# Kernel optimization log

Measured on AMD Instinct MI355X. Metric: run time of the kernel, lower is better.

The kernel has to match this reference:

```python
import jax, jax.numpy as jnp
import numpy as np
from jax import lax

B, T = 64, 200
NUM_C, DIM_S, SIZE_M = 2000, 128, 50


def setup_inputs() -> dict:
    key = jax.random.key(0)
    ks = jax.random.split(key, 12)
    d = {}
    d['skill'] = jax.random.randint(ks[0], (B, T), 0, NUM_C)
    d['answer'] = jax.random.randint(ks[1], (B, T), 0, 2)
    s = 1.0 / np.sqrt(DIM_S)
    d['k_emb'] = jax.random.normal(ks[2], (NUM_C + 1, DIM_S), jnp.float32)
    d['v_emb'] = jax.random.normal(ks[3], (2 * NUM_C + 1, DIM_S), jnp.float32)
    # kaiming_normal on [size_m, dim_s]: std = sqrt(2/dim_s)
    d['Mk'] = jax.random.normal(ks[4], (SIZE_M, DIM_S), jnp.float32) * np.sqrt(2.0 / DIM_S)
    d['Mv0'] = jax.random.normal(ks[5], (SIZE_M, DIM_S), jnp.float32) * np.sqrt(2.0 / DIM_S)
    d['f_W'] = jax.random.normal(ks[6], (DIM_S, 2 * DIM_S), jnp.float32) * (1.0 / np.sqrt(2 * DIM_S))
    d['f_b'] = jnp.zeros((DIM_S,), jnp.float32)
    d['p_W'] = jax.random.normal(ks[7], (NUM_C, DIM_S), jnp.float32) * s
    d['p_b'] = jnp.zeros((NUM_C,), jnp.float32)
    d['e_W'] = jax.random.normal(ks[8], (DIM_S, DIM_S), jnp.float32) * s
    d['e_b'] = jnp.zeros((DIM_S,), jnp.float32)
    d['a_W'] = jax.random.normal(ks[9], (DIM_S, DIM_S), jnp.float32) * s
    d['a_b'] = jnp.zeros((DIM_S,), jnp.float32)
    return d


def reference(skill, answer, k_emb, v_emb, Mk, Mv0, f_W, f_b, p_W, p_b, e_W, e_b, a_W, a_b):
    num_c = p_W.shape[0]
    bsz = skill.shape[0]
    answer_x = jnp.where(answer == 2, 1, answer)
    x = skill + num_c * answer_x                       # [B,T]
    k = k_emb[skill]                                   # [B,T,D]
    v = v_emb[x]                                       # [B,T,D]
    w = jax.nn.softmax(jnp.einsum('btd,md->btm', k, Mk), axis=-1)   # [B,T,M]
    e = jax.nn.sigmoid(jnp.einsum('btd,ed->bte', v, e_W) + e_b)      # [B,T,D]
    a = jnp.tanh(jnp.einsum('btd,ed->bte', v, a_W) + a_b)            # [B,T,D]

    Mv_init = jnp.broadcast_to(Mv0, (bsz,) + Mv0.shape)              # [B,M,D]

    def step(Mvt, inp):
        et, at, wt = inp                               # [B,D],[B,D],[B,M]
        # read uses pre-update memory (Mv[:, :-1] in the torch code)
        read = jnp.einsum('bm,bmd->bd', wt, Mvt)
        Mvt_new = Mvt * (1.0 - wt[:, :, None] * et[:, None, :]) + wt[:, :, None] * at[:, None, :]
        return Mvt_new, read

    _, reads = lax.scan(step, Mv_init,
                        (e.transpose(1, 0, 2), a.transpose(1, 0, 2), w.transpose(1, 0, 2)))
    reads = reads.transpose(1, 0, 2)                   # [B,T,D]

    f = jnp.tanh(jnp.concatenate([reads, k], axis=-1) @ f_W.T + f_b)  # [B,T,D]
    p = jax.nn.sigmoid(f @ p_W.T + p_b)                # [B,T,num_c] (dropout is identity at eval)
    p = p[:, :-1, :]
    next_skill = skill[:, 1:]                          # [B,T-1]
    idx = jnp.minimum(next_skill, num_c - 1)
    pred = jnp.take_along_axis(p, idx[..., None], axis=-1)[..., 0]
    pred = jnp.where(next_skill < num_c, pred, 0.0)    # index num_c -> zero row in torch one_hot
    return pred
```

## Files before the change

kernel.cpp:

```cpp
#include <hip/hip_runtime.h>
#include <math.h>

#define Bsz 64
#define Tn 200
#define NUMC 2000
#define DS 128
#define SM 50
#define NTOK (Bsz*Tn)
#define WVS 10
#define CH 40
#define NCH (Tn/CH)

typedef __attribute__((ext_vector_type(8))) short bfrag;
typedef __attribute__((ext_vector_type(4))) float f32x4;
typedef __attribute__((ext_vector_type(4))) unsigned int u32x4;

__device__ __forceinline__ unsigned short f2bf(float x) {
    unsigned int u = __builtin_bit_cast(unsigned int, x);
    u = u + 0x7fffu + ((u >> 16) & 1u);
    return (unsigned short)(u >> 16);
}
__device__ __forceinline__ unsigned int pack2(float a, float b) {
    return (unsigned int)f2bf(a) | ((unsigned int)f2bf(b) << 16);
}
__device__ __forceinline__ bfrag mk_frag(f32x4 x, f32x4 y) {
    u32x4 t;
    t[0] = pack2(x[0], x[1]); t[1] = pack2(x[2], x[3]);
    t[2] = pack2(y[0], y[1]); t[3] = pack2(y[2], y[3]);
    return __builtin_bit_cast(bfrag, t);
}

__device__ __forceinline__ float fast_exp(float x)  { return __builtin_amdgcn_exp2f(x * 1.44269504f); }
__device__ __forceinline__ float fast_rcp(float x)  { return __builtin_amdgcn_rcpf(x); }
__device__ __forceinline__ float fast_sigmoid(float x) { return fast_rcp(1.f + fast_exp(-x)); }
__device__ __forceinline__ float fast_tanh(float x) { return 1.f - 2.f * fast_rcp(fast_exp(2.f * x) + 1.f); }

__global__ __launch_bounds__(256) void k0_cast(
    const float* __restrict__ eW, const float* __restrict__ aW,
    const float* __restrict__ fW, const float* __restrict__ Mk,
    unsigned int* __restrict__ BeaU, unsigned int* __restrict__ BkmU,
    unsigned int* __restrict__ Bf0U)
{
    const int g = blockIdx.x * 256 + threadIdx.x;
    if (g >= 9216) return;
    int gm, mat;
    unsigned int* dst;
    if (g < 4096)      { mat = 0; gm = g;        dst = BeaU; }
    else if (g < 7168) { mat = 1; gm = g - 4096; dst = BkmU; }
    else               { mat = 2; gm = g - 7168; dst = Bf0U; }
    const int nt = gm >> 8, r = gm & 255, ki = r >> 6, L = r & 63;
    const int n = nt * 16 + (L & 15);
    const int k = ki * 32 + (L >> 4) * 8;

    const float* src = nullptr;
    if (mat == 0) {
        src = (n < 128) ? (eW + (size_t)n * DS + k) : (aW + (size_t)(n - 128) * DS + k);
    } else if (mat == 1) {
        if (n < 128)      src = fW + (size_t)n * (2 * DS) + DS + k;
        else if (n < 128 + SM) src = Mk + (size_t)(n - 128) * DS + k;
    } else {
        src = fW + (size_t)n * (2 * DS) + k;
    }
    float v[8];
    #pragma unroll
    for (int j = 0; j < 8; j++) v[j] = src ? src[j] : 0.f;
    u32x4 o;
    o[0] = pack2(v[0], v[1]); o[1] = pack2(v[2], v[3]);
    o[2] = pack2(v[4], v[5]); o[3] = pack2(v[6], v[7]);
    ((u32x4*)dst)[gm] = o;
}

__global__ __launch_bounds__(64, 4) void k1_gemm(
    const int* __restrict__ skill, const int* __restrict__ answer,
    const float* __restrict__ k_emb, const float* __restrict__ v_emb,
    const unsigned int* __restrict__ BeaU, const unsigned int* __restrict__ BkmU,
    const float* __restrict__ eB, const float* __restrict__ aB,
    float* __restrict__ w_buf, float* __restrict__ e_buf,
    float* __restrict__ a_buf, float* __restrict__ kp_buf)
{
    const int bid = blockIdx.x;
    const int tile = bid / 7, role = bid % 7;
    const int L = threadIdx.x, L15 = L & 15, quad = L >> 4;
    const int tok0 = tile * 16;
    const int tokA = tok0 + L15;
    const int row0 = tok0 + quad * 4;

    const int s = skill[tokA];
    const float* ap;
    if (role < 4) {
        const int an = answer[tokA];
        const int ax = (an == 2) ? 1 : an;
        ap = v_emb + ((size_t)(s + NUMC * ax)) * DS + quad * 8;
    } else {
        ap = k_emb + (size_t)s * DS + quad * 8;
    }
    bfrag Af[4];
    #pragma unroll
    for (int ki = 0; ki < 4; ki++) {
        const f32x4* a4 = (const f32x4*)(ap + ki * 32);
        Af[ki] = mk_frag(a4[0], a4[1]);
    }

    const bfrag* Bp = (role < 4) ? (const bfrag*)BeaU : (const bfrag*)BkmU;
    const int g0 = (role < 4) ? role * 4 : (role - 4) * 4;

    f32x4 acc[4];
    #pragma unroll
    for (int t = 0; t < 4; t++) acc[t] = (f32x4){0.f,0.f,0.f,0.f};

    #pragma unroll
    for (int half = 0; half < 2; half++) {
        bfrag bh[2][4];
        #pragma unroll
        for (int tt = 0; tt < 2; tt++)
            #pragma unroll
            for (int ki = 0; ki < 4; ki++)
                bh[tt][ki] = Bp[(size_t)((g0 + half * 2 + tt) * 4 + ki) * 64 + L];
        #pragma unroll
        for (int ki = 0; ki < 4; ki++)
            #pragma unroll
            for (int tt = 0; tt < 2; tt++)
                acc[half * 2 + tt] = __builtin_amdgcn_mfma_f32_16x16x32_bf16(
                    Af[ki], bh[tt][ki], acc[half * 2 + tt], 0, 0, 0);
    }

    if (role == 6) {
        #pragma unroll
        for (int reg = 0; reg < 4; reg++) {
            float mx = -1e30f;
            #pragma unroll
            for (int t = 0; t < 4; t++) { const int c = t * 16 + L15; if (c < SM) mx = fmaxf(mx, acc[t][reg]); }
            #pragma unroll
            for (int msk = 1; msk <= 8; msk <<= 1) mx = fmaxf(mx, __shfl_xor(mx, msk));
            float ex[4]; float ssum = 0.f;
            #pragma unroll
            for (int t = 0; t < 4; t++) {
                const int c = t * 16 + L15;
                ex[t] = (c < SM) ? fast_exp(acc[t][reg] - mx) : 0.f;
                ssum += ex[t];
            }
            #pragma unroll
            for (int msk = 1; msk <= 8; msk <<= 1) ssum += __shfl_xor(ssum, msk);
            const float inv = fast_rcp(ssum);
            float* wp = w_buf + (size_t)(row0 + reg) * SM;
            #pragma unroll
            for (int t = 0; t < 4; t++) { const int c = t * 16 + L15; if (c < SM) wp[c] = ex[t] * inv; }
        }
    } else {
        const int nb = (role & 1) * 64;
        float* obuf = (role < 2) ? e_buf : (role < 4) ? a_buf : kp_buf;
        const float* bias = (role < 2) ? eB : aB;
        #pragma unroll
        for (int t = 0; t < 4; t++) {
            const int n = nb + t * 16 + L15;
            const float bv = (role < 4) ? bias[n] : 0.f;
            #pragma unroll
            for (int reg = 0; reg < 4; reg++) {
                float v = acc[t][reg] + bv;
                if (role < 2)      v = fast_sigmoid(v);
                else if (role < 4) v = fast_tanh(v);
                obuf[(size_t)(row0 + reg) * DS + n] = v;
            }
        }
    }
}

__global__ __launch_bounds__(640) void k2_scan(
    const float* __restrict__ w_buf, const float* __restrict__ e_buf,
    const float* __restrict__ a_buf, const float* __restrict__ Mv0,
    unsigned short* __restrict__ reads)
{
    const int bi   = blockIdx.x;
    const int b    = bi >> 1;
    const int dh   = bi & 1;
    const int tid  = threadIdx.x;
    const int wv   = tid >> 6;
    const int L    = tid & 63;
    const int d    = dh * 64 + L;
    const int m0e  = wv * 5;
    const int base = b * Tn;

    __shared__ float se_s[2][CH][64];
    __shared__ float sa_s[2][CH][64];
    __shared__ float sw_s[2][CH * SM];
    __shared__ float red[2][WVS][8][64];

    float Mv[5];
    #pragma unroll
    for (int m = 0; m < 5; m++) Mv[m] = Mv0[(size_t)(m0e + m) * DS + d];

    const int r0 = tid >> 6, c0 = tid & 63;

    {
        const size_t ebase = (size_t)base * DS + dh * 64 + c0;
        #pragma unroll
        for (int pp = 0; pp < 4; pp++) {
            const int row = pp * 10 + r0;
            se_s[0][row][c0] = e_buf[ebase + (size_t)row * DS];
            sa_s[0][row][c0] = a_buf[ebase + (size_t)row * DS];
        }
        const int wbase = base * SM;
        #pragma unroll
        for (int pp = 0; pp < 4; pp++) {
            const int j = tid + pp * 640;
            if (j < CH * SM) sw_s[0][j] = w_buf[wbase + j];
        }
    }
    __syncthreads();

    float se[4][2], sa[4][2], sw[4][2][5];
    int p = 0;

    #define LOADST(ST, TL)                                                     \
        { const int tl_ = (TL);                                                \
          if (tl_ < CH) {                                                      \
            _Pragma("unroll")                                                  \
            for (int q_ = 0; q_ < 2; q_++) {                                   \
                se[ST][q_] = se_s[p][tl_ + q_][L];                             \
                sa[ST][q_] = sa_s[p][tl_ + q_][L];                             \
                _Pragma("unroll")                                              \
                for (int m_ = 0; m_ < 5; m_++)                                 \
                    sw[ST][q_][m_] = sw_s[p][(tl_ + q_) * SM + m0e + m_];      \
            } } }

    for (int c = 0; c < NCH; c++) {
        float st_e[4], st_a[4], st_w[4];
        if (c + 1 < NCH) {
            const int tcn = (c + 1) * CH;
            const size_t ebase = (size_t)(base + tcn) * DS + dh * 64 + c0;
            #pragma unroll
            for (int pp = 0; pp < 4; pp++) {
                const int row = pp * 10 + r0;
                st_e[pp] = e_buf[ebase + (size_t)row * DS];
                st_a[pp] = a_buf[ebase + (size_t)row * DS];
            }
            const int wbase = (base + tcn) * SM;
            #pragma unroll
            for (int pp = 0; pp < 4; pp++) {
                const int j = tid + pp * 640;
                if (j < CH * SM) st_w[pp] = w_buf[wbase + j];
            }
        }

        LOADST(0, 0) LOADST(1, 2) LOADST(2, 4) LOADST(3, 6)

        #pragma unroll 1
        for (int ti = 0; ti < 5; ti++) {
            const int tlb = ti * 8;
            const int gi  = c * 5 + ti;
            const int pr  = gi & 1;
            #pragma unroll
            for (int sub = 0; sub < 4; sub++) {
                #pragma unroll
                for (int q = 0; q < 2; q++) {
                    const float ev = se[sub][q], av = sa[sub][q];
                    float rd = 0.f;
                    #pragma unroll
                    for (int m = 0; m < 5; m++) {
                        const float wm = sw[sub][q][m];
                        rd = fmaf(wm, Mv[m], rd);
                        Mv[m] = fmaf(-wm, fmaf(ev, Mv[m], -av), Mv[m]);
                    }
                    red[pr][wv][sub * 2 + q][L] = rd;
                }
                LOADST(sub, tlb + sub * 2 + 8)
            }
            __syncthreads();
            if (tid < 512) {
                const int tt = tid >> 6, dd = tid & 63;
                float s = red[pr][0][tt][dd];
                #pragma unroll
                for (int g = 1; g < WVS; g++) s += red[pr][g][tt][dd];
                reads[(size_t)(base + c * CH + tlb + tt) * DS + dh * 64 + dd] = f2bf(s);
            }
        }

        if (c + 1 < NCH) {
            #pragma unroll
            for (int pp = 0; pp < 4; pp++) {
                const int row = pp * 10 + r0;
                se_s[p ^ 1][row][c0] = st_e[pp];
                sa_s[p ^ 1][row][c0] = st_a[pp];
            }
            #pragma unroll
            for (int pp = 0; pp < 4; pp++) {
                const int j = tid + pp * 640;
                if (j < CH * SM) sw_s[p ^ 1][j] = st_w[pp];
            }
            __syncthreads();
            p ^= 1;
        }
    }
    #undef LOADST
}

__global__ __launch_bounds__(128, 2) void k3_gemm(
    const unsigned short* __restrict__ reads, const float* __restrict__ kp_buf,
    const unsigned int* __restrict__ Bf0U, const float* __restrict__ fB,
    const float* __restrict__ pW, const float* __restrict__ pB,
    const int* __restrict__ skill, float* __restrict__ out)
{
    const int tid = threadIdx.x;
    const int wv  = tid >> 6;
    const int L   = tid & 63, L15 = L & 15, quad = L >> 4;
    const int tok0 = blockIdx.x * 16;
    const int tokA = tok0 + L15;
    const int row0 = tok0 + quad * 4;

    __shared__ float sm[2][16];

    bfrag Rf[4];
    #pragma unroll
    for (int ki = 0; ki < 4; ki++)
        Rf[ki] = *(const bfrag*)(reads + (size_t)tokA * DS + ki * 32 + quad * 8);

    const bfrag* Bf0 = (const bfrag*)Bf0U;
    const int g0 = wv * 4;

    f32x4 acc[4];
    #pragma unroll
    for (int t = 0; t < 4; t++) acc[t] = (f32x4){0.f,0.f,0.f,0.f};

    #pragma unroll
    for (int half = 0; half < 2; half++) {
        bfrag bh[2][4];
        #pragma unroll
        for (int tt = 0; tt < 2; tt++)
            #pragma unroll
            for (int ki = 0; ki < 4; ki++)
                bh[tt][ki] = Bf0[(size_t)((g0 + half * 2 + tt) * 4 + ki) * 64 + L];
        #pragma unroll
        for (int ki = 0; ki < 4; ki++)
            #pragma unroll
            for (int tt = 0; tt < 2; tt++)
                acc[half * 2 + tt] = __builtin_amdgcn_mfma_f32_16x16x32_bf16(
                    Rf[ki], bh[tt][ki], acc[half * 2 + tt], 0, 0, 0);
    }

    const int nb = wv * 64;
    float f[4][4];
    #pragma unroll
    for (int t = 0; t < 4; t++) {
        const int n = nb + t * 16 + L15;
        const float fb = fB[n];
        #pragma unroll
        for (int reg = 0; reg < 4; reg++)
            f[reg][t] = fast_tanh(acc[t][reg] + kp_buf[(size_t)(row0 + reg) * DS + n] + fb);
    }

    #pragma unroll
    for (int reg = 0; reg < 4; reg++) {
        const int tok = row0 + reg;
        const int t = tok % Tn;
        const bool act = (t < Tn - 1);
        float contrib = 0.f;
        if (act) {
            const int sn = skill[tok + 1];
            const int ix = (sn < NUMC) ? sn : (NUMC - 1);
            const float* pr = pW + (size_t)ix * DS + nb + L15;
            #pragma unroll
            for (int t4 = 0; t4 < 4; t4++)
                contrib = fmaf(f[reg][t4], pr[t4 * 16], contrib);
        }
        #pragma unroll
        for (int msk = 1; msk <= 8; msk <<= 1)
            contrib += __shfl_xor(contrib, msk);
        if (L15 == 0) sm[wv][quad * 4 + reg] = contrib;
    }
    __syncthreads();
    if (tid < 16) {
        const int tok = tok0 + tid;
        const int t = tok % Tn;
        if (t < Tn - 1) {
            const int sn = skill[tok + 1];
            const int ix = (sn < NUMC) ? sn : (NUMC - 1);
            const float val = sm[0][tid] + sm[1][tid] + pB[ix];
            out[(size_t)(tok / Tn) * (Tn - 1) + t] = (sn < NUMC) ? fast_sigmoid(val) : 0.f;
        }
    }
}

extern "C" void kernel_launch(void* const* d_in, const int* in_sizes, int n_in,
                              void* d_out, int out_size, void* d_ws, size_t ws_size,
                              hipStream_t stream)
{
    const int*   skill  = (const int*)  d_in[0];
    const int*   answer = (const int*)  d_in[1];
    const float* k_emb  = (const float*)d_in[2];
    const float* v_emb  = (const float*)d_in[3];
    const float* Mk     = (const float*)d_in[4];
    const float* Mv0    = (const float*)d_in[5];
    const float* f_W    = (const float*)d_in[6];
    const float* f_b    = (const float*)d_in[7];
    const float* p_W    = (const float*)d_in[8];
    const float* p_b    = (const float*)d_in[9];
    const float* e_W    = (const float*)d_in[10];
    const float* e_b    = (const float*)d_in[11];
    const float* a_W    = (const float*)d_in[12];
    const float* a_b    = (const float*)d_in[13];
    float* out = (float*)d_out;

    float* ws     = (float*)d_ws;
    float* w_buf  = ws;
    float* e_buf  = w_buf  + (size_t)NTOK*SM;
    float* a_buf  = e_buf  + (size_t)NTOK*DS;
    float* kp_buf = a_buf  + (size_t)NTOK*DS;
    unsigned short* reads = (unsigned short*)(kp_buf + (size_t)NTOK*DS);
    unsigned int* BeaU = (unsigned int*)(reads + (size_t)NTOK*DS);
    unsigned int* BkmU = BeaU + 4096 * 4;
    unsigned int* Bf0U = BkmU + 3072 * 4;

    k0_cast<<<36, 256, 0, stream>>>(e_W, a_W, f_W, Mk, BeaU, BkmU, Bf0U);
    k1_gemm<<<7*(NTOK/16), 64, 0, stream>>>(skill, answer, k_emb, v_emb,
        BeaU, BkmU, e_b, a_b, w_buf, e_buf, a_buf, kp_buf);
    k2_scan<<<Bsz*2, 640, 0, stream>>>(w_buf, e_buf, a_buf, Mv0, reads);
    k3_gemm<<<NTOK/16, 128, 0, stream>>>(reads, kp_buf, Bf0U, f_b,
        p_W, p_b, skill, out);
}
```

Before: 138.9 us.

## Halve scan block to 5 waves with 10 memory slots each and vectorized LDS

The recurrent scan kernel now uses 320 threads per block, each wave owning 10 memory slots instead of 5. This halves the cross-wave reduction and the number of threads synchronizing each step. Shared buffers are transposed and padded so e, a and w values can be read as vector loads. The reduction also writes packed bf16 pairs. The cost is twice the serial FMA work per thread and more registers per thread.

```diff
diff --git a/kernel.cpp b/kernel.cpp
--- a/kernel.cpp
+++ b/kernel.cpp
@@ -7,12 +7,16 @@
 #define DS 128
 #define SM 50
 #define NTOK (Bsz*Tn)
-#define WVS 10
+#define WVS2 5
+#define MPW 10
 #define CH 40
 #define NCH (Tn/CH)
+#define SEP 44
+#define WROW 60
 
 typedef __attribute__((ext_vector_type(8))) short bfrag;
 typedef __attribute__((ext_vector_type(4))) float f32x4;
+typedef __attribute__((ext_vector_type(2))) float f32x2;
 typedef __attribute__((ext_vector_type(4))) unsigned int u32x4;
 
 __device__ __forceinline__ unsigned short f2bf(float x) {
@@ -165,7 +169,7 @@
     }
 }
 
-__global__ __launch_bounds__(640) void k2_scan(
+__global__ __launch_bounds__(320) void k2_scan(
     const float* __restrict__ w_buf, const float* __restrict__ e_buf,
     const float* __restrict__ a_buf, const float* __restrict__ Mv0,
     unsigned short* __restrict__ reads)
@@ -177,121 +181,130 @@
     const int wv   = tid >> 6;
     const int L    = tid & 63;
     const int d    = dh * 64 + L;
-    const int m0e  = wv * 5;
+    const int m0   = wv * MPW;
     const int base = b * Tn;
 
-    __shared__ float se_s[2][CH][64];
-    __shared__ float sa_s[2][CH][64];
-    __shared__ float sw_s[2][CH * SM];
-    __shared__ float red[2][WVS][8][64];
-
-    float Mv[5];
-    #pragma unroll
-    for (int m = 0; m < 5; m++) Mv[m] = Mv0[(size_t)(m0e + m) * DS + d];
-
-    const int r0 = tid >> 6, c0 = tid & 63;
+    __shared__ __align__(16) float se_s[2][64][SEP];
+    __shared__ __align__(16) float sa_s[2][64][SEP];
+    __shared__ __align__(16) float w_s[2][CH][WROW];
+    __shared__ __align__(16) float red[2][WVS2][8][64];
+
+    float Mv[MPW];
+    #pragma unroll
+    for (int m = 0; m < MPW; m++) Mv[m] = Mv0[(size_t)(m0 + m) * DS + d];
+
+    const int srow = tid >> 6, scol = tid & 63;
 
     {
-        const size_t ebase = (size_t)base * DS + dh * 64 + c0;
-        #pragma unroll
-        for (int pp = 0; pp < 4; pp++) {
-            const int row = pp * 10 + r0;
-            se_s[0][row][c0] = e_buf[ebase + (size_t)row * DS];
-            sa_s[0][row][c0] = a_buf[ebase + (size_t)row * DS];
-        }
-        const int wbase = base * SM;
-        #pragma unroll
-        for (int pp = 0; pp < 4; pp++) {
-            const int j = tid + pp * 640;
-            if (j < CH * SM) sw_s[0][j] = w_buf[wbase + j];
+        #pragma unroll
+        for (int pass = 0; pass < 8; pass++) {
+            const int row = pass * 5 + srow;
+            se_s[0][scol][row] = e_buf[(size_t)(base + row) * DS + dh * 64 + scol];
+            sa_s[0][scol][row] = a_buf[(size_t)(base + row) * DS + dh * 64 + scol];
+        }
+        #pragma unroll
+        for (int pass = 0; pass < 7; pass++) {
+            const int j = tid + pass * 320;
+            if (j < CH * SM) {
+                const int t = j / SM, m = j % SM;
+                w_s[0][t][(m / MPW) * 12 + (m % MPW)] = w_buf[(size_t)base * SM + j];
+            }
         }
     }
     __syncthreads();
 
-    float se[4][2], sa[4][2], sw[4][2][5];
+    f32x4 wlo[2][2], whi[2][2];
+    f32x2 wtl[2][2], sev[2], sav[2];
     int p = 0;
 
-    #define LOADST(ST, TL)                                                     \
+    #define LOADR(SL, TL)                                                      \
         { const int tl_ = (TL);                                                \
           if (tl_ < CH) {                                                      \
+            sev[SL] = *(const f32x2*)&se_s[p][L][tl_];                         \
+            sav[SL] = *(const f32x2*)&sa_s[p][L][tl_];                         \
             _Pragma("unroll")                                                  \
             for (int q_ = 0; q_ < 2; q_++) {                                   \
-                se[ST][q_] = se_s[p][tl_ + q_][L];                             \
-                sa[ST][q_] = sa_s[p][tl_ + q_][L];                             \
-                _Pragma("unroll")                                              \
-                for (int m_ = 0; m_ < 5; m_++)                                 \
-                    sw[ST][q_][m_] = sw_s[p][(tl_ + q_) * SM + m0e + m_];      \
+                const float* wp_ = &w_s[p][tl_ + q_][wv * 12];                 \
+                wlo[SL][q_] = *(const f32x4*)wp_;                              \
+                whi[SL][q_] = *(const f32x4*)(wp_ + 4);                        \
+                wtl[SL][q_] = *(const f32x2*)(wp_ + 8);                        \
             } } }
 
+    LOADR(0, 0) LOADR(1, 2)
+
     for (int c = 0; c < NCH; c++) {
-        float st_e[4], st_a[4], st_w[4];
+        float st_e[8], st_a[8], st_w[7];
         if (c + 1 < NCH) {
-            const int tcn = (c + 1) * CH;
-            const size_t ebase = (size_t)(base + tcn) * DS + dh * 64 + c0;
-            #pragma unroll
-            for (int pp = 0; pp < 4; pp++) {
-                const int row = pp * 10 + r0;
-                st_e[pp] = e_buf[ebase + (size_t)row * DS];
-                st_a[pp] = a_buf[ebase + (size_t)row * DS];
-            }
-            const int wbase = (base + tcn) * SM;
-            #pragma unroll
-            for (int pp = 0; pp < 4; pp++) {
-                const int j = tid + pp * 640;
-                if (j < CH * SM) st_w[pp] = w_buf[wbase + j];
-            }
-        }
-
-        LOADST(0, 0) LOADST(1, 2) LOADST(2, 4) LOADST(3, 6)
+            const int t0n = (c + 1) * CH;
+            #pragma unroll
+            for (int pass = 0; pass < 8; pass++) {
+                const int row = pass * 5 + srow;
+                st_e[pass] = e_buf[(size_t)(base + t0n + row) * DS + dh * 64 + scol];
+                st_a[pass] = a_buf[(size_t)(base + t0n + row) * DS + dh * 64 + scol];
+            }
+            #pragma unroll
+            for (int pass = 0; pass < 7; pass++) {
+                const int j = tid + pass * 320;
+                st_w[pass] = (j < CH * SM) ? w_buf[(size_t)(base + t0n) * SM + j] : 0.f;
+            }
+        }
 
         #pragma unroll 1
         for (int ti = 0; ti < 5; ti++) {
             const int tlb = ti * 8;
-            const int gi  = c * 5 + ti;
-            const int pr  = gi & 1;
-            #pragma unroll
-            for (int sub = 0; sub < 4; sub++) {
+            const int pr  = (c * 5 + ti) & 1;
+            #pragma unroll
+            for (int s = 0; s < 4; s++) {
+                const int slot = s & 1;
                 #pragma unroll
                 for (int q = 0; q < 2; q++) {
-                    const float ev = se[sub][q], av = sa[sub][q];
+                    const float ev = sev[slot][q], av = sav[slot][q];
                     float rd = 0.f;
                     #pragma unroll
-                    for (int m = 0; m < 5; m++) {
-                        const float wm = sw[sub][q][m];
+                    for (int m = 0; m < MPW; m++) {
+                        const float wm = (m < 4) ? wlo[slot][q][m]
+                                       : (m < 8) ? whi[slot][q][m - 4]
+                                                 : wtl[slot][q][m - 8];
                         rd = fmaf(wm, Mv[m], rd);
                         Mv[m] = fmaf(-wm, fmaf(ev, Mv[m], -av), Mv[m]);
                     }
-                    red[pr][wv][sub * 2 + q][L] = rd;
+                    red[pr][wv][s * 2 + q][L] = rd;
                 }
-                LOADST(sub, tlb + sub * 2 + 8)
+                LOADR(slot, tlb + s * 2 + 4)
             }
             __syncthreads();
-            if (tid < 512) {
-                const int tt = tid >> 6, dd = tid & 63;
-                float s = red[pr][0][tt][dd];
+            if (tid < 256) {
+                const int tt = tid >> 5, dd2 = tid & 31;
+                f32x2 s2 = *(const f32x2*)&red[pr][0][tt][dd2 * 2];
                 #pragma unroll
-                for (int g = 1; g < WVS; g++) s += red[pr][g][tt][dd];
-                reads[(size_t)(base + c * CH + tlb + tt) * DS + dh * 64 + dd] = f2bf(s);
+                for (int g = 1; g < WVS2; g++)
+                    s2 += *(const f32x2*)&red[pr][g][tt][dd2 * 2];
+                *(unsigned int*)&reads[(size_t)(base + c * CH + tlb + tt) * DS + dh * 64 + dd2 * 2]
+                    = pack2(s2[0], s2[1]);
             }
         }
 
         if (c + 1 < NCH) {
             #pragma unroll
-            for (int pp = 0; pp < 4; pp++) {
-                const int row = pp * 10 + r0;
-                se_s[p ^ 1][row][c0] = st_e[pp];
-                sa_s[p ^ 1][row][c0] = st_a[pp];
-            }
-            #pragma unroll
-            for (int pp = 0; pp < 4; pp++) {
-                const int j = tid + pp * 640;
-                if (j < CH * SM) sw_s[p ^ 1][j] = st_w[pp];
+            for (int pass = 0; pass < 8; pass++) {
+                const int row = pass * 5 + srow;
+                se_s[p ^ 1][scol][row] = st_e[pass];
+                sa_s[p ^ 1][scol][row] = st_a[pass];
+            }
+            #pragma unroll
+            for (int pass = 0; pass < 7; pass++) {
+                const int j = tid + pass * 320;
+                if (j < CH * SM) {
+                    const int t = j / SM, m = j % SM;
+                    w_s[p ^ 1][t][(m / MPW) * 12 + (m % MPW)] = st_w[pass];
+                }
             }
             __syncthreads();
             p ^= 1;
-        }
-    }
-    #undef LOADST
+            LOADR(0, 0) LOADR(1, 2)
+        }
+    }
+    #undef LOADR
 }
 
 __global__ __launch_bounds__(128, 2) void k3_gemm(
@@ -413,7 +426,7 @@
     k0_cast<<<36, 256, 0, stream>>>(e_W, a_W, f_W, Mk, BeaU, BkmU, Bf0U);
     k1_gemm<<<7*(NTOK/16), 64, 0, stream>>>(skill, answer, k_emb, v_emb,
         BeaU, BkmU, e_b, a_b, w_buf, e_buf, a_buf, kp_buf);
-    k2_scan<<<Bsz*2, 640, 0, stream>>>(w_buf, e_buf, a_buf, Mv0, reads);
+    k2_scan<<<Bsz*2, 320, 0, stream>>>(w_buf, e_buf, a_buf, Mv0, reads);
     k3_gemm<<<NTOK/16, 128, 0, stream>>>(reads, kp_buf, Bf0U, f_b,
         p_W, p_b, skill, out);
 }
```

New measurement: 141.5 us. Within noise of the previous version (+1.9%).
